# Kernel optimization log

Measured on AMD Instinct MI355X. Metric: run time of the kernel, lower is better.

Reference implementation:

```python
import jax, jax.numpy as jnp
import numpy as np

NUM_MIRNA = 20000
NUM_GENE = 30000
N = NUM_MIRNA + NUM_GENE  # 50000 homogeneous nodes
R = 4                      # num_relations
E = 1000000                # num edges
IN_C, HID, OUT, NB = 128, 128, 64, 10


def setup_inputs() -> dict:
    key = jax.random.key(0)
    ks = jax.random.split(key, 20)
    s = 0.05
    inp = {}
    inp["x_mirna"] = jax.random.normal(ks[0], (NUM_MIRNA, 256), jnp.float32)
    inp["x_gene"] = jax.random.normal(ks[1], (NUM_GENE, 512), jnp.float32)
    inp["edge_index"] = jax.random.randint(ks[2], (2, E), 0, N)
    inp["edge_type"] = jax.random.randint(ks[3], (E,), 0, R)
    # per-node-type input projections
    inp["lin_w_m"] = jax.random.normal(ks[4], (256, IN_C), jnp.float32) * s
    inp["lin_b_m"] = jnp.zeros((IN_C,), jnp.float32)
    inp["lin_w_g"] = jax.random.normal(ks[5], (512, IN_C), jnp.float32) * s
    inp["lin_b_g"] = jnp.zeros((IN_C,), jnp.float32)
    # RGCNConv layer 1 (basis decomposition)
    inp["comp1"] = jax.random.normal(ks[6], (R, NB), jnp.float32) * s
    inp["basis1"] = jax.random.normal(ks[7], (NB, IN_C, HID), jnp.float32) * s
    inp["root1"] = jax.random.normal(ks[8], (IN_C, HID), jnp.float32) * s
    inp["bias1"] = jnp.zeros((HID,), jnp.float32)
    # RGCNConv layer 2
    inp["comp2"] = jax.random.normal(ks[9], (R, NB), jnp.float32) * s
    inp["basis2"] = jax.random.normal(ks[10], (NB, HID, OUT), jnp.float32) * s
    inp["root2"] = jax.random.normal(ks[11], (HID, OUT), jnp.float32) * s
    inp["bias2"] = jnp.zeros((OUT,), jnp.float32)
    return inp


def rgcn_conv(x, src, dst, etype, comp, basis, root, bias):
    # W_r = sum_b comp[r,b] * basis[b] : [R, I, O]
    W = jnp.einsum('rb,bio->rio', comp, basis)
    # transform every node under every relation: [R, N, O]
    h = jnp.einsum('ni,rio->rno', x, W)
    # gather per-edge message from (relation, source) pair: [E, O]
    msg = h[etype, src]
    # per-(relation, dst) mean aggregation (PyG RGCNConv aggr='mean')
    seg = etype * N + dst
    summed = jax.ops.segment_sum(msg, seg, num_segments=R * N)
    cnt = jax.ops.segment_sum(jnp.ones((msg.shape[0],), msg.dtype), seg,
                              num_segments=R * N)
    mean = summed / jnp.maximum(cnt, 1.0)[:, None]
    agg = mean.reshape(R, N, -1).sum(0)  # sum over relations
    return agg + x @ root + bias


def reference(x_mirna, x_gene, edge_index, edge_type,
              lin_w_m, lin_b_m, lin_w_g, lin_b_g,
              comp1, basis1, root1, bias1,
              comp2, basis2, root2, bias2):
    xm = x_mirna @ lin_w_m + lin_b_m
    xg = x_gene @ lin_w_g + lin_b_g
    x = jnp.concatenate([xm, xg], axis=0)  # to_homogeneous, miRNA first
    src, dst = edge_index[0], edge_index[1]
    x = rgcn_conv(x, src, dst, edge_type, comp1, basis1, root1, bias1)
    x = rgcn_conv(x, src, dst, edge_type, comp2, basis2, root2, bias2)
    return x[:NUM_MIRNA], x[NUM_MIRNA:]
```

## Files before the change

kernel.cpp:

```cpp
#include <hip/hip_runtime.h>
#include <hip/hip_bf16.h>

#define NUM_MIRNA 20000
#define NUM_GENE  30000
#define NN        50000
#define RR        4
#define EE        1000000
#define IN_C      128
#define HIDC      128
#define OUTC      64
#define NBASIS    10
#define NSEG      (RR * NN)
#define NSEGP     200704
#define KFUSE     640
#define SROW      512

#define NBKT   256
#define BSH    8
#define NBKTU  ((NN + 255) >> 8)
#define CHUNK  4096
#define NCHUNK ((EE + CHUNK - 1) / CHUNK)

typedef __attribute__((ext_vector_type(8))) short bf16x8;
typedef __attribute__((ext_vector_type(4))) float f32x4;
typedef __attribute__((ext_vector_type(2))) float f32x2;

__device__ inline ushort f2bf(float x) {
    uint u = __float_as_uint(x);
    uint r = u + 0x7fffu + ((u >> 16) & 1u);
    return (ushort)(r >> 16);
}
__device__ inline uint pack2bf(float lo, float hi) {
    return (uint)f2bf(lo) | ((uint)f2bf(hi) << 16);
}
__device__ inline f32x2 up2(uint u) {
    return (f32x2){__uint_as_float(u << 16), __uint_as_float(u & 0xffff0000u)};
}

#define GLOAD_LDS16(gsrc, ldst)                                                \
    __builtin_amdgcn_global_load_lds(                                          \
        (const __attribute__((address_space(1))) void*)(gsrc),                 \
        (__attribute__((address_space(3))) void*)(ldst), 16, 0, 0)

__global__ void tcast_k(const float* __restrict__ W, ushort* __restrict__ Wt,
                        int K, int OC) {
    int idx = blockIdx.x * 256 + threadIdx.x;
    if (idx >= K * OC) return;
    int o = idx / K, k = idx % K;
    Wt[idx] = f2bf(W[(size_t)k * OC + o]);
}

__global__ void buildW_k(const float* __restrict__ comp, const float* __restrict__ basis,
                         const float* __restrict__ root, ushort* __restrict__ Wt, int O) {
    int idx = blockIdx.x * 256 + threadIdx.x;
    if (idx >= O * KFUSE) return;
    int o = idx / KFUSE, k = idx % KFUSE;
    float acc;
    if (k < 512) {
        int r = k >> 7, i = k & 127;
        acc = 0.f;
#pragma unroll
        for (int b = 0; b < NBASIS; ++b)
            acc += comp[r * NBASIS + b] * basis[((size_t)b * 128 + i) * O + o];
    } else {
        acc = root[(size_t)(k - 512) * O + o];
    }
    Wt[idx] = f2bf(acc);
}

template <int NT, int K, bool OUT_BF16, bool ROOTX, bool A_F32>
__global__ __launch_bounds__(256) void sgemm_k(
    const void* __restrict__ Av, const ushort* __restrict__ xroot,
    const ushort* __restrict__ Wt, const float* __restrict__ bias,
    void* __restrict__ Cout, int M)
{
    constexpr int OC = 2 * NT * 16;
    constexpr int BK = 64;
    constexpr int NTILE = K / BK;
    constexpr int AS = ROOTX ? SROW : K;
    const ushort* A  = (const ushort*)Av;
    const float*  Af = (const float*)Av;

    __shared__ __align__(16) ushort As[2 * 4096];

    const int tid  = threadIdx.x;
    const int lane = tid & 63;
    const int wid  = tid >> 6;
    const int wm   = wid >> 1;
    const int wn   = wid & 1;
    const int l15  = lane & 15;
    const int lg   = lane >> 4;
    const int rowBase = blockIdx.x * 64;
    const int colBase = wn * NT * 16;

    f32x4 acc[2][NT];
#pragma unroll
    for (int mt = 0; mt < 2; ++mt)
#pragma unroll
        for (int nt = 0; nt < NT; ++nt)
            acc[mt][nt] = (f32x4){0.f, 0.f, 0.f, 0.f};

    auto STAGE = [&](int buf, int t) {
        const int kc = t * BK;
#pragma unroll
        for (int i = 0; i < 2; ++i) {
            int L   = i * 4096 + tid * 16;
            int row = L >> 7;
            int bs  = (L & 127) ^ ((row & 7) << 4);
            int grow = rowBase + row; if (grow >= M) grow = M - 1;
            if (A_F32) {
                const float* src = Af + (size_t)grow * K + kc + (bs >> 1);
                float4 f0 = *(const float4*)src;
                float4 f1 = *(const float4*)(src + 4);
                bf16x8 tv;
                tv[0] = (short)f2bf(f0.x); tv[1] = (short)f2bf(f0.y);
                tv[2] = (short)f2bf(f0.z); tv[3] = (short)f2bf(f0.w);
                tv[4] = (short)f2bf(f1.x); tv[5] = (short)f2bf(f1.y);
                tv[6] = (short)f2bf(f1.z); tv[7] = (short)f2bf(f1.w);
                *(bf16x8*)&As[(size_t)buf * 4096 + (L >> 1)] = tv;
            } else {
                const ushort* src;
                if (!ROOTX || kc < SROW)
                    src = A + (size_t)grow * AS + kc + (bs >> 1);
                else
                    src = xroot + (size_t)grow * IN_C + (kc - SROW) + (bs >> 1);
                GLOAD_LDS16(src, &As[(size_t)buf * 4096 + (L >> 1)]);
            }
        }
    };

    STAGE(0, 0);
    __syncthreads();

#pragma unroll
    for (int t = 0; t < NTILE; ++t) {
        const int kc  = t * BK;
        const int buf = t & 1;

        bf16x8 bB[2][NT];
#pragma unroll
        for (int kk = 0; kk < 2; ++kk)
#pragma unroll
            for (int nt = 0; nt < NT; ++nt)
                bB[kk][nt] = *(const bf16x8*)(
                    Wt + (size_t)(colBase + nt * 16 + l15) * K + kc + kk * 32 + lg * 8);

        if (t + 1 < NTILE) STAGE(buf ^ 1, t + 1);

        bf16x8 aF[2][2];
#pragma unroll
        for (int mt = 0; mt < 2; ++mt)
#pragma unroll
            for (int kk = 0; kk < 2; ++kk) {
                int row = wm * 32 + mt * 16 + l15;
                int kb  = kk * 64 + lg * 16;
                aF[mt][kk] = *(const bf16x8*)&As[
                    (size_t)buf * 4096 + row * 64 + ((kb ^ ((row & 7) << 4)) >> 1)];
            }

#pragma unroll
        for (int kk = 0; kk < 2; ++kk)
#pragma unroll
            for (int nt = 0; nt < NT; ++nt)
#pragma unroll
                for (int mt = 0; mt < 2; ++mt)
                    acc[mt][nt] = __builtin_amdgcn_mfma_f32_16x16x32_bf16(
                        aF[mt][kk], bB[kk][nt], acc[mt][nt], 0, 0, 0);

        __syncthreads();
    }

#pragma unroll
    for (int nt = 0; nt < NT; ++nt) {
        int n = colBase + nt * 16 + l15;
        float bv = bias ? bias[n] : 0.f;
#pragma unroll
        for (int mt = 0; mt < 2; ++mt) {
#pragma unroll
            for (int q = 0; q < 4; ++q) {
                int m = rowBase + wm * 32 + mt * 16 + lg * 4 + q;
                if (m < M) {
                    float v = acc[mt][nt][q] + bv;
                    size_t off = (size_t)m * OC + n;
                    if (OUT_BF16) ((ushort*)Cout)[off] = f2bf(v);
                    else          ((float*)Cout)[off]  = v;
                }
            }
        }
    }
}

__global__ __launch_bounds__(256) void bs0_k(const int* __restrict__ dstA,
                                             int* __restrict__ bcnt) {
    __shared__ int h[NBKT];
    int t = threadIdx.x;
    h[t] = 0;
    __syncthreads();
    int e0 = blockIdx.x * CHUNK;
    int n = EE - e0; if (n > CHUNK) n = CHUNK;
    for (int i = t; i < n; i += 256)
        atomicAdd(&h[dstA[e0 + i] >> BSH], 1);
    __syncthreads();
    if (h[t]) atomicAdd(&bcnt[t], h[t]);
}

__global__ void bscan_k(const int* __restrict__ bcnt, int* __restrict__ bbase,
                        int* __restrict__ bcur) {
    __shared__ int sm[NBKT];
    int t = threadIdx.x;
    int v = bcnt[t];
    sm[t] = v; __syncthreads();
    for (int off = 1; off < NBKT; off <<= 1) {
        int x = (t >= off) ? sm[t - off] : 0;
        __syncthreads();
        sm[t] += x;
        __syncthreads();
    }
    int ex = sm[t] - v;
    bbase[t] = ex;
    bcur[t]  = ex;
}

__global__ __launch_bounds__(256) void bs1_k(const int* __restrict__ srcA,
                                             const int* __restrict__ dstA,
                                             const int* __restrict__ et,
                                             int* __restrict__ bcur,
                                             uint* __restrict__ bpay) {
    __shared__ int h[NBKT], cur[NBKT], boff[NBKT];
    __shared__ uint lpay[CHUNK];
    __shared__ unsigned char lbkt[CHUNK];
    int t = threadIdx.x;
    h[t] = 0; cur[t] = 0;
    __syncthreads();
    int e0 = blockIdx.x * CHUNK;
    int n = EE - e0; if (n > CHUNK) n = CHUNK;
    for (int i = t; i < n; i += 256) {
        int e = e0 + i;
        int d = dstA[e];
        int s2 = d * 4 + et[e];
        int b = d >> BSH;
        lpay[i] = ((uint)(s2 & 1023) << 17) | (uint)srcA[e];
        lbkt[i] = (unsigned char)b;
        atomicAdd(&h[b], 1);
    }
    __syncthreads();
    if (h[t]) boff[t] = atomicAdd(&bcur[t], h[t]);
    __syncthreads();
    for (int i = t; i < n; i += 256) {
        int b = lbkt[i];
        int slot = atomicAdd(&cur[b], 1);
        bpay[boff[b] + slot] = lpay[i];
    }
}

__global__ __launch_bounds__(256) void sortbkt_k(
    const uint* __restrict__ bpay, const int* __restrict__ bbase,
    const int* __restrict__ bcnt, int* __restrict__ sorted,
    int* __restrict__ cnt, int* __restrict__ base, float* __restrict__ inv)
{
    __shared__ int hist[1024];
    __shared__ int tsum[256];
    const int b = blockIdx.x;
    const int t = threadIdx.x;
    const int segbase = b << 10;

#pragma unroll
    for (int i = 0; i < 4; ++i) hist[t + i * 256] = 0;
    __syncthreads();

    const int e0 = bbase[b];
    const int n  = bcnt[b];
    for (int i = t; i < n; i += 256)
        atomicAdd(&hist[(int)(bpay[e0 + i] >> 17)], 1);
    __syncthreads();

    int h0 = hist[t * 4], h1 = hist[t * 4 + 1], h2 = hist[t * 4 + 2], h3 = hist[t * 4 + 3];
    int s = h0 + h1 + h2 + h3;
    tsum[t] = s; __syncthreads();
    for (int off = 1; off < 256; off <<= 1) {
        int x = (t >= off) ? tsum[t - off] : 0;
        __syncthreads();
        tsum[t] += x;
        __syncthreads();
    }
    int run = (t > 0) ? tsum[t - 1] : 0;
    int b0 = run, b1 = run + h0, b2 = b1 + h1, b3 = b2 + h2;

    ((int4*)cnt)[(segbase >> 2) + t]  = make_int4(h0, h1, h2, h3);
    ((int4*)base)[(segbase >> 2) + t] = make_int4(e0 + b0, e0 + b1, e0 + b2, e0 + b3);
    ((float4*)inv)[(segbase >> 2) + t] = make_float4(
        1.0f / fmaxf((float)h0, 1.0f), 1.0f / fmaxf((float)h1, 1.0f),
        1.0f / fmaxf((float)h2, 1.0f), 1.0f / fmaxf((float)h3, 1.0f));

    hist[t * 4] = b0; hist[t * 4 + 1] = b1; hist[t * 4 + 2] = b2; hist[t * 4 + 3] = b3;
    __syncthreads();

    for (int i = t; i < n; i += 256) {
        uint val = bpay[e0 + i];
        int pos = atomicAdd(&hist[(int)(val >> 17)], 1);
        sorted[e0 + pos] = (int)((val & 0x1FFFFu) << 8);
    }
}

__global__ __launch_bounds__(256) void gatherS_k(
    const ushort* __restrict__ x, const int* __restrict__ sorted,
    const int* __restrict__ base, const int* __restrict__ cnt,
    const float* __restrict__ inv, ushort* __restrict__ S)
{
    int d = (blockIdx.x * 256 + threadIdx.x) >> 6;
    int lane = threadIdx.x & 63;
    if (d >= NN) return;
    const char* xb = (const char*)x;
    uint4* Sp = (uint4*)S;
    const int slot = lane >> 4;
    const int cg   = lane & 15;
    const int cgb  = cg << 4;

    int4   b4 = ((const int4*)base)[d];
    int4   c4 = ((const int4*)cnt)[d];
    float4 w4 = ((const float4*)inv)[d];
    const int ofr[4]  = {0, b4.y - b4.x, b4.z - b4.x, b4.w - b4.x};
    const int cnts[4] = {c4.x, c4.y, c4.z, c4.w};
    const float wts[4] = {w4.x, w4.y, w4.z, w4.w};
    const int tot = (b4.w + c4.w) - b4.x;

    f32x2 acc[4][4];
#pragma unroll
    for (int r = 0; r < 4; ++r)
#pragma unroll
        for (int t = 0; t < 4; ++t) acc[r][t] = (f32x2){0.f, 0.f};

    if (tot <= 64) {
        int idx = sorted[b4.x + lane];
        int maxn = max(max(cnts[0], cnts[1]), max(cnts[2], cnts[3]));
        for (int j = 0; j < maxn; j += 4) {
            int e = j + slot;
#pragma unroll
            for (int r = 0; r < 4; ++r) {
                int off = __shfl(idx, ofr[r] + e);
                if (e < cnts[r]) {
                    uint4 v = *(const uint4*)(xb + off + cgb);
                    acc[r][0] += up2(v.x);
                    acc[r][1] += up2(v.y);
                    acc[r][2] += up2(v.z);
                    acc[r][3] += up2(v.w);
                }
            }
        }
    } else {
#pragma unroll
        for (int r = 0; r < 4; ++r) {
            int s0 = b4.x + ofr[r];
            int s1 = s0 + cnts[r];
            for (int i0 = s0; i0 < s1; i0 += 64) {
                int idx2 = sorted[i0 + lane];
                int n2 = s1 - i0; if (n2 > 64) n2 = 64;
                for (int j = 0; j < n2; j += 4) {
                    int e = j + slot;
                    int off = __shfl(idx2, e);
                    if (e < n2) {
                        uint4 v = *(const uint4*)(xb + off + cgb);
                        acc[r][0] += up2(v.x);
                        acc[r][1] += up2(v.y);
                        acc[r][2] += up2(v.z);
                        acc[r][3] += up2(v.w);
                    }
                }
            }
        }
    }

#pragma unroll
    for (int r = 0; r < 4; ++r) {
        float wt = wts[r];
#pragma unroll
        for (int t = 0; t < 4; ++t) {
            acc[r][t].x += __shfl_xor(acc[r][t].x, 16);
            acc[r][t].y += __shfl_xor(acc[r][t].y, 16);
            acc[r][t].x += __shfl_xor(acc[r][t].x, 32);
            acc[r][t].y += __shfl_xor(acc[r][t].y, 32);
        }
        if (slot == 0) {
            uint4 o;
            o.x = pack2bf(acc[r][0].x * wt, acc[r][0].y * wt);
            o.y = pack2bf(acc[r][1].x * wt, acc[r][1].y * wt);
            o.z = pack2bf(acc[r][2].x * wt, acc[r][2].y * wt);
            o.w = pack2bf(acc[r][3].x * wt, acc[r][3].y * wt);
            Sp[(size_t)d * 64 + r * 16 + cg] = o;
        }
    }
}

extern "C" void kernel_launch(void* const* d_in, const int* in_sizes, int n_in,
                              void* d_out, int out_size, void* d_ws, size_t ws_size,
                              hipStream_t stream) {
    const float* x_mirna = (const float*)d_in[0];
    const float* x_gene  = (const float*)d_in[1];
    const int*   eidx    = (const int*)d_in[2];
    const int*   etype   = (const int*)d_in[3];
    const float* lin_w_m = (const float*)d_in[4];
    const float* lin_b_m = (const float*)d_in[5];
    const float* lin_w_g = (const float*)d_in[6];
    const float* lin_b_g = (const float*)d_in[7];
    const float* comp1   = (const float*)d_in[8];
    const float* basis1  = (const float*)d_in[9];
    const float* root1   = (const float*)d_in[10];
    const float* bias1   = (const float*)d_in[11];
    const float* comp2   = (const float*)d_in[12];
    const float* basis2  = (const float*)d_in[13];
    const float* root2   = (const float*)d_in[14];
    const float* bias2   = (const float*)d_in[15];

    const int* srcA = eidx;
    const int* dstA = eidx + EE;

    char* p = (char*)d_ws;
    ushort* x0bf = (ushort*)p; p += (size_t)(NN + 1) * IN_C * 2;
    ushort* x1bf = (ushort*)p; p += (size_t)(NN + 1) * HIDC * 2;
    ushort* S    = (ushort*)p; p += (size_t)NN * SROW * 2;
    ushort* Wtm  = (ushort*)p; p += (size_t)IN_C * 256 * 2;
    ushort* Wtg  = (ushort*)p; p += (size_t)IN_C * 512 * 2;
    ushort* Wt1s = (ushort*)p; p += (size_t)HIDC * KFUSE * 2;
    ushort* Wt2s = (ushort*)p; p += (size_t)OUTC * KFUSE * 2;
    float* inv   = (float*)p;  p += (size_t)NSEGP * 4;
    int* cnt     = (int*)p;    p += (size_t)NSEGP * 4;
    int* base    = (int*)p;    p += (size_t)NSEGP * 4;
    int* bcnt    = (int*)p;    p += NBKT * 4;
    int* bbase   = (int*)p;    p += NBKT * 4;
    int* bcur    = (int*)p;    p += NBKT * 4;
    int* sorted  = (int*)p;    p += (size_t)(EE + 64) * 4;
    uint* bpay   = (uint*)p;   p += (size_t)EE * 4;

    float* outp = (float*)d_out;

    hipMemsetAsync(bcnt, 0, NBKT * sizeof(int), stream);

    tcast_k<<<(256 * IN_C + 255) / 256, 256, 0, stream>>>(lin_w_m, Wtm, 256, IN_C);
    tcast_k<<<(512 * IN_C + 255) / 256, 256, 0, stream>>>(lin_w_g, Wtg, 512, IN_C);
    buildW_k<<<(HIDC * KFUSE + 255) / 256, 256, 0, stream>>>(comp1, basis1, root1, Wt1s, HIDC);
    buildW_k<<<(OUTC * KFUSE + 255) / 256, 256, 0, stream>>>(comp2, basis2, root2, Wt2s, OUTC);

    bs0_k<<<NCHUNK, 256, 0, stream>>>(dstA, bcnt);
    bscan_k<<<1, NBKT, 0, stream>>>(bcnt, bbase, bcur);
    bs1_k<<<NCHUNK, 256, 0, stream>>>(srcA, dstA, etype, bcur, bpay);
    sortbkt_k<<<NBKTU, 256, 0, stream>>>(bpay, bbase, bcnt, sorted, cnt, base, inv);

    sgemm_k<4, 256, true, false, true><<<dim3((NUM_MIRNA + 63) / 64), 256, 0, stream>>>(
        x_mirna, nullptr, Wtm, lin_b_m, x0bf, NUM_MIRNA);
    sgemm_k<4, 512, true, false, true><<<dim3((NUM_GENE + 63) / 64), 256, 0, stream>>>(
        x_gene, nullptr, Wtg, lin_b_g, x0bf + (size_t)NUM_MIRNA * IN_C, NUM_GENE);

    gatherS_k<<<(NN * 64 + 255) / 256, 256, 0, stream>>>(x0bf, sorted, base, cnt, inv, S);
    sgemm_k<4, KFUSE, true, true, false><<<dim3((NN + 63) / 64), 256, 0, stream>>>(
        S, x0bf, Wt1s, bias1, x1bf, NN);

    gatherS_k<<<(NN * 64 + 255) / 256, 256, 0, stream>>>(x1bf, sorted, base, cnt, inv, S);
    sgemm_k<2, KFUSE, false, true, false><<<dim3((NN + 63) / 64), 256, 0, stream>>>(
        S, x1bf, Wt2s, bias2, outp, NN);
}
```

Measured before the change: 273.6 us.

## Fuse weight-prep kernels and prefetch fp32 A tiles into registers across MFMA

```diff
diff --git a/kernel.cpp b/kernel.cpp
--- a/kernel.cpp
+++ b/kernel.cpp
@@ -42,30 +42,51 @@
         (const __attribute__((address_space(1))) void*)(gsrc),                 \
         (__attribute__((address_space(3))) void*)(ldst), 16, 0, 0)
 
-__global__ void tcast_k(const float* __restrict__ W, ushort* __restrict__ Wt,
-                        int K, int OC) {
-    int idx = blockIdx.x * 256 + threadIdx.x;
-    if (idx >= K * OC) return;
-    int o = idx / K, k = idx % K;
-    Wt[idx] = f2bf(W[(size_t)k * OC + o]);
-}
-
-__global__ void buildW_k(const float* __restrict__ comp, const float* __restrict__ basis,
-                         const float* __restrict__ root, ushort* __restrict__ Wt, int O) {
-    int idx = blockIdx.x * 256 + threadIdx.x;
-    if (idx >= O * KFUSE) return;
-    int o = idx / KFUSE, k = idx % KFUSE;
-    float acc;
-    if (k < 512) {
-        int r = k >> 7, i = k & 127;
-        acc = 0.f;
-#pragma unroll
-        for (int b = 0; b < NBASIS; ++b)
-            acc += comp[r * NBASIS + b] * basis[((size_t)b * 128 + i) * O + o];
-    } else {
-        acc = root[(size_t)(k - 512) * O + o];
-    }
-    Wt[idx] = f2bf(acc);
+__global__ void prep_k(const float* __restrict__ lin_w_m, const float* __restrict__ lin_w_g,
+                       const float* __restrict__ comp1, const float* __restrict__ basis1,
+                       const float* __restrict__ root1,
+                       const float* __restrict__ comp2, const float* __restrict__ basis2,
+                       const float* __restrict__ root2,
+                       ushort* __restrict__ Wtm, ushort* __restrict__ Wtg,
+                       ushort* __restrict__ Wt1s, ushort* __restrict__ Wt2s) {
+    int gidx = blockIdx.x * 256 + threadIdx.x;
+    if (gidx < 32768) {
+        int idx = gidx;
+        int o = idx >> 8, k = idx & 255;
+        Wtm[idx] = f2bf(lin_w_m[(size_t)k * IN_C + o]);
+    } else if (gidx < 98304) {
+        int idx = gidx - 32768;
+        int o = idx >> 9, k = idx & 511;
+        Wtg[idx] = f2bf(lin_w_g[(size_t)k * IN_C + o]);
+    } else if (gidx < 180224) {
+        int idx = gidx - 98304;
+        int o = idx / KFUSE, k = idx % KFUSE;
+        float acc;
+        if (k < 512) {
+            int r = k >> 7, i = k & 127;
+            acc = 0.f;
+#pragma unroll
+            for (int b = 0; b < NBASIS; ++b)
+                acc += comp1[r * NBASIS + b] * basis1[((size_t)b * 128 + i) * HIDC + o];
+        } else {
+            acc = root1[(size_t)(k - 512) * HIDC + o];
+        }
+        Wt1s[idx] = f2bf(acc);
+    } else if (gidx < 221184) {
+        int idx = gidx - 180224;
+        int o = idx / KFUSE, k = idx % KFUSE;
+        float acc;
+        if (k < 512) {
+            int r = k >> 7, i = k & 127;
+            acc = 0.f;
+#pragma unroll
+            for (int b = 0; b < NBASIS; ++b)
+                acc += comp2[r * NBASIS + b] * basis2[((size_t)b * 128 + i) * OUTC + o];
+        } else {
+            acc = root2[(size_t)(k - 512) * OUTC + o];
+        }
+        Wt2s[idx] = f2bf(acc);
+    }
 }
 
 template <int NT, int K, bool OUT_BF16, bool ROOTX, bool A_F32>
@@ -100,6 +121,8 @@
         for (int nt = 0; nt < NT; ++nt)
             acc[mt][nt] = (f32x4){0.f, 0.f, 0.f, 0.f};
 
+    float4 fA[2][2];
+
     auto STAGE = [&](int buf, int t) {
         const int kc = t * BK;
 #pragma unroll
@@ -108,28 +131,43 @@
             int row = L >> 7;
             int bs  = (L & 127) ^ ((row & 7) << 4);
             int grow = rowBase + row; if (grow >= M) grow = M - 1;
-            if (A_F32) {
-                const float* src = Af + (size_t)grow * K + kc + (bs >> 1);
-                float4 f0 = *(const float4*)src;
-                float4 f1 = *(const float4*)(src + 4);
-                bf16x8 tv;
-                tv[0] = (short)f2bf(f0.x); tv[1] = (short)f2bf(f0.y);
-                tv[2] = (short)f2bf(f0.z); tv[3] = (short)f2bf(f0.w);
-                tv[4] = (short)f2bf(f1.x); tv[5] = (short)f2bf(f1.y);
-                tv[6] = (short)f2bf(f1.z); tv[7] = (short)f2bf(f1.w);
-                *(bf16x8*)&As[(size_t)buf * 4096 + (L >> 1)] = tv;
-            } else {
-                const ushort* src;
-                if (!ROOTX || kc < SROW)
-                    src = A + (size_t)grow * AS + kc + (bs >> 1);
-                else
-                    src = xroot + (size_t)grow * IN_C + (kc - SROW) + (bs >> 1);
-                GLOAD_LDS16(src, &As[(size_t)buf * 4096 + (L >> 1)]);
-            }
+            const ushort* src;
+            if (!ROOTX || kc < SROW)
+                src = A + (size_t)grow * AS + kc + (bs >> 1);
+            else
+                src = xroot + (size_t)grow * IN_C + (kc - SROW) + (bs >> 1);
+            GLOAD_LDS16(src, &As[(size_t)buf * 4096 + (L >> 1)]);
         }
     };
-
-    STAGE(0, 0);
+    auto STAGE_LOAD = [&](int t) {
+        const int kc = t * BK;
+#pragma unroll
+        for (int i = 0; i < 2; ++i) {
+            int L   = i * 4096 + tid * 16;
+            int row = L >> 7;
+            int bs  = (L & 127) ^ ((row & 7) << 4);
+            int grow = rowBase + row; if (grow >= M) grow = M - 1;
+            const float* src = Af + (size_t)grow * K + kc + (bs >> 1);
+            fA[i][0] = *(const float4*)src;
+            fA[i][1] = *(const float4*)(src + 4);
+        }
+    };
+    auto STAGE_WRITE = [&](int buf) {
+#pragma unroll
+        for (int i = 0; i < 2; ++i) {
+            int L = i * 4096 + tid * 16;
+            float4 f0 = fA[i][0], f1 = fA[i][1];
+            bf16x8 tv;
+            tv[0] = (short)f2bf(f0.x); tv[1] = (short)f2bf(f0.y);
+            tv[2] = (short)f2bf(f0.z); tv[3] = (short)f2bf(f0.w);
+            tv[4] = (short)f2bf(f1.x); tv[5] = (short)f2bf(f1.y);
+            tv[6] = (short)f2bf(f1.z); tv[7] = (short)f2bf(f1.w);
+            *(bf16x8*)&As[(size_t)buf * 4096 + (L >> 1)] = tv;
+        }
+    };
+
+    if (A_F32) { STAGE_LOAD(0); STAGE_WRITE(0); }
+    else       STAGE(0, 0);
     __syncthreads();
 
 #pragma unroll
@@ -145,7 +183,10 @@
                 bB[kk][nt] = *(const bf16x8*)(
                     Wt + (size_t)(colBase + nt * 16 + l15) * K + kc + kk * 32 + lg * 8);
 
-        if (t + 1 < NTILE) STAGE(buf ^ 1, t + 1);
+        if (t + 1 < NTILE) {
+            if (A_F32) STAGE_LOAD(t + 1);
+            else       STAGE(buf ^ 1, t + 1);
+        }
 
         bf16x8 aF[2][2];
 #pragma unroll
@@ -167,6 +208,7 @@
                     acc[mt][nt] = __builtin_amdgcn_mfma_f32_16x16x32_bf16(
                         aF[mt][kk], bB[kk][nt], acc[mt][nt], 0, 0, 0);
 
+        if (A_F32 && t + 1 < NTILE) STAGE_WRITE(buf ^ 1);
         __syncthreads();
     }
 
@@ -435,10 +477,9 @@
 
     hipMemsetAsync(bcnt, 0, NBKT * sizeof(int), stream);
 
-    tcast_k<<<(256 * IN_C + 255) / 256, 256, 0, stream>>>(lin_w_m, Wtm, 256, IN_C);
-    tcast_k<<<(512 * IN_C + 255) / 256, 256, 0, stream>>>(lin_w_g, Wtg, 512, IN_C);
-    buildW_k<<<(HIDC * KFUSE + 255) / 256, 256, 0, stream>>>(comp1, basis1, root1, Wt1s, HIDC);
-    buildW_k<<<(OUTC * KFUSE + 255) / 256, 256, 0, stream>>>(comp2, basis2, root2, Wt2s, OUTC);
+    prep_k<<<(221184 + 255) / 256, 256, 0, stream>>>(
+        lin_w_m, lin_w_g, comp1, basis1, root1, comp2, basis2, root2,
+        Wtm, Wtg, Wt1s, Wt2s);
 
     bs0_k<<<NCHUNK, 256, 0, stream>>>(dstA, bcnt);
     bscan_k<<<1, NBKT, 0, stream>>>(bcnt, bbase, bcur);
```

Result: faster. 265.8 us (-2.9%).
